# Optimization experiments

Measured on AMD Instinct MI355X. Metric: run time of the kernel, lower is better.

The kernel has to match this reference:

```python
import jax, jax.numpy as jnp
import numpy as np

B, T, LBL = 256, 1024, 128  # batch, seq_len, label_size (incl. start/end)
NUM = LBL - 2               # real emission labels


def setup_inputs() -> dict:
    key = jax.random.key(0)
    k1, k2, k3, k4 = jax.random.split(key, 4)
    logits = jax.random.normal(k1, (B, T, NUM), jnp.float32)
    labels = jax.random.randint(k2, (B, T), 0, NUM)
    lens = jax.random.randint(k3, (B,), 1, T + 1)  # 1..T inclusive
    transition = jax.random.normal(k4, (LBL, LBL), jnp.float32)
    # CRF.initialize(): nothing may transition INTO start-row source or OUT of end
    transition = transition.at[:, LBL - 1].set(-100.0)
    transition = transition.at[LBL - 2, :].set(-100.0)
    return {"logits": logits, "labels": labels, "lens": lens, "transition": transition}


def reference(logits, labels, lens, transition):
    """CRF negative-free log-likelihood pieces: returns gold_score - norm_score per sequence ([B])."""
    Bb, Tt, num = logits.shape
    L = transition.shape[0]
    start, end = L - 2, L - 1

    # pad_logits: append two -1000 columns for start/end labels -> [B, T, L]
    pads = jnp.full((Bb, Tt, 2), -1000.0, logits.dtype)
    lg = jnp.concatenate([logits, pads], axis=2)

    # ---- gold unary score ----
    mask_t = jnp.arange(Tt)[None, :] < lens[:, None]            # [B, T]
    unary = jnp.take_along_axis(lg, labels[..., None], axis=2)[..., 0]
    unary = jnp.where(mask_t, unary, 0.0).sum(axis=1)

    # ---- gold binary (transition) score ----
    ext = jnp.concatenate(
        [jnp.full((Bb, 1), start, labels.dtype), labels,
         jnp.full((Bb, 1), end, labels.dtype)], axis=1)          # [B, T+2]
    mask_e = jnp.arange(Tt + 2)[None, :] < (lens + 1)[:, None]
    ext = jnp.where(mask_e, ext, end)                            # positions >= len+1 -> end
    trn_scr = transition[ext[:, 1:], ext[:, :-1]]                # [B, T+1] (row=next, col=prev)
    mask_b = jnp.arange(Tt + 1)[None, :] < (lens + 1)[:, None]
    binary = jnp.where(mask_b, trn_scr, 0.0).sum(axis=1)

    gold = unary + binary

    # ---- partition (norm) score via log-sum-exp scan over time ----
    alpha0 = jnp.full((Bb, L), -100.0, lg.dtype).at[:, start].set(0.0)
    lg_t = jnp.transpose(lg, (1, 0, 2))                          # [T, B, L]

    def step(alpha, xs):
        logit, t = xs                                            # logit: [B, L]
        # mat[b, j, i] = logit[b, j] + alpha[b, i] + transition[j, i]
        mat = logit[:, :, None] + alpha[:, None, :] + transition[None]
        alpha_nxt = jax.nn.logsumexp(mat, axis=2)                # [B, L]
        alpha = jnp.where((t < lens)[:, None], alpha_nxt, alpha)
        return alpha, None

    alpha, _ = jax.lax.scan(step, alpha0, (lg_t, jnp.arange(Tt)))
    alpha = alpha + transition[end][None, :]
    norm = jax.nn.logsumexp(alpha, axis=1)                       # [B]

    return gold - norm
```

## Files before the change

### kernel.cpp

```cpp
#include <hip/hip_runtime.h>


typedef _Float16 half_t;
typedef _Float16 h2 __attribute__((ext_vector_type(2)));
typedef _Float16 h8 __attribute__((ext_vector_type(8)));

#define TB  1024
#define NUM 126
#define LBL 128

__device__ __forceinline__ float dot2(h2 a, h2 b, float c) {
  return __builtin_amdgcn_fdot2(a, b, c, false);
}

template <int U>
__device__ __forceinline__ float dotu(h8 a, h8 e, float c) {
  return dot2(__builtin_shufflevector(a, a, 2 * U, 2 * U + 1),
              __builtin_shufflevector(e, e, 2 * U, 2 * U + 1), c);
}

template <int CTRL>
__device__ __forceinline__ float dpp_max_step(float x) {
  int xi = __float_as_int(x);
  int yi = __builtin_amdgcn_update_dpp(xi, xi, CTRL, 0xF, 0xF, false);
  return fmaxf(x, __int_as_float(yi));
}

__device__ __forceinline__ float wave_max64(float x) {
  x = dpp_max_step<0x111>(x);
  x = dpp_max_step<0x112>(x);
  x = dpp_max_step<0x114>(x);
  x = dpp_max_step<0x118>(x);
  x = dpp_max_step<0x142>(x);
  x = dpp_max_step<0x143>(x);
  return __int_as_float(__builtin_amdgcn_readlane(__float_as_int(x), 63));
}

__global__ __launch_bounds__(64, 1)
void crf_fwd(const float* __restrict__ logits, const int* __restrict__ labels,
             const int* __restrict__ lens, const float* __restrict__ trans,
             float* __restrict__ out)
{
  const int b  = blockIdx.x;
  const int l  = threadIdx.x;
  const int j0 = l;
  const int j1 = l + 64;
  const int off1 = (j1 < NUM) ? j1 : (NUM - 1);
  const float mask1 = (j1 < NUM) ? 1.0f : 0.0f;
  const int len = lens[b];

  __shared__ h2 a_sh[64];
  h8* a_sh8 = (h8*)a_sh;

  const float* lgbase = logits + (size_t)b * TB * NUM;
  const int*   lab    = labels + (size_t)b * TB;

  h8 E0[16], E1[16];
  {
    const float* tr0 = trans + j0 * LBL;
    const float* tr1 = trans + j1 * LBL;
    #pragma unroll
    for (int q = 0; q < 16; ++q) {
      h8 v0, v1;
      #pragma unroll
      for (int e = 0; e < 8; ++e) {
        int p = 8 * q + e;
        int i = (p >> 1) + 64 * (p & 1);
        v0[e] = (half_t)__expf(tr0[i]);
        v1[e] = (half_t)__expf(tr1[i]);
      }
      E0[q] = v0; E1[q] = v1;
    }
  }

  float g = 0.f;
  #pragma unroll
  for (int kk = 0; kk < 16; ++kk) {
    int t = l + 64 * kk;
    if (t < len) {
      int lt = lab[t];
      int lp = (t == 0) ? (LBL - 2) : lab[t - 1];
      g += lgbase[(size_t)t * NUM + lt] + trans[lt * LBL + lp];
    }
  }
  if (l == 0) g += trans[(LBL - 1) * LBL + lab[len - 1]];
  #pragma unroll
  for (int o = 1; o < 64; o <<= 1) g += __shfl_xor(g, o);
  const float gold = g;

  {
    h2 a_init;
    a_init[0] = (half_t)0.0f;
    a_init[1] = (half_t)((j1 == LBL - 2) ? 1.0f : 0.0f);
    a_sh[l] = a_init;
  }

  float plg0[4], plg1[4];
  #pragma unroll
  for (int d = 0; d < 4; ++d) {
    plg0[d] = lgbase[(size_t)d * NUM + j0];
    plg1[d] = lgbase[(size_t)d * NUM + off1];
  }

  int   P    = 6;
  int   Kacc = 0;
  int   Kout = 0;
  float w0_out = 1.f, w1_out = 1.f;

#define STEP_BODY(Q0, Q1)                                                   \
  {                                                                         \
    float eL0 = __expf(Q0);                                                 \
    float eL1 = __expf(Q1) * mask1;                                         \
    float s0a = 0.f, s0b = 0.f, s1a = 0.f, s1b = 0.f;                       \
    _Pragma("unroll")                                                       \
    for (int q = 0; q < 16; q += 2) {                                       \
      h8 avA = a_sh8[q], avB = a_sh8[q + 1];    \
      h8 e0A = E0[q], e0B = E0[q + 1], e1A = E1[q], e1B = E1[q + 1];        \
      s0a = dotu<0>(avA, e0A, s0a);  s0b = dotu<0>(avB, e0B, s0b);          \
      s1a = dotu<0>(avA, e1A, s1a);  s1b = dotu<0>(avB, e1B, s1b);          \
      s0a = dotu<1>(avA, e0A, s0a);  s0b = dotu<1>(avB, e0B, s0b);          \
      s1a = dotu<1>(avA, e1A, s1a);  s1b = dotu<1>(avB, e1B, s1b);          \
      s0a = dotu<2>(avA, e0A, s0a);  s0b = dotu<2>(avB, e0B, s0b);          \
      s1a = dotu<2>(avA, e1A, s1a);  s1b = dotu<2>(avB, e1B, s1b);          \
      s0a = dotu<3>(avA, e0A, s0a);  s0b = dotu<3>(avB, e0B, s0b);          \
      s1a = dotu<3>(avA, e1A, s1a);  s1b = dotu<3>(avB, e1B, s1b);          \
    }                                                                       \
    float w0 = (s0a + s0b) * eL0;                                           \
    float w1 = (s1a + s1b) * eL1;                                           \
    float sc = __int_as_float((127 - P) << 23);      \
    h2 pk;                                                                  \
    pk[0] = (half_t)(w0 * sc);                                              \
    pk[1] = (half_t)(w1 * sc);                                              \
    a_sh[l] = pk;                        \
    Kout = Kacc;  Kacc += P;                           \
    \
    float m  = wave_max64(fmaxf(w0, w1));                                   \
    int   Em = ((__float_as_int(m) >> 23) & 0xFF) - 127;                    \
    P = Em - P + 6;                   \
    w0_out = w0; w1_out = w1;                                               \
  }

  int t = 0;
  for (; t + 4 <= len; t += 4) {
    int r0 = t + 4, r1 = t + 5, r2 = t + 6, r3 = t + 7;
    r0 = (r0 < TB) ? r0 : (TB - 1);  r1 = (r1 < TB) ? r1 : (TB - 1);
    r2 = (r2 < TB) ? r2 : (TB - 1);  r3 = (r3 < TB) ? r3 : (TB - 1);
    STEP_BODY(plg0[0], plg1[0])
    plg0[0] = lgbase[(size_t)r0 * NUM + j0];
    plg1[0] = lgbase[(size_t)r0 * NUM + off1];
    STEP_BODY(plg0[1], plg1[1])
    plg0[1] = lgbase[(size_t)r1 * NUM + j0];
    plg1[1] = lgbase[(size_t)r1 * NUM + off1];
    STEP_BODY(plg0[2], plg1[2])
    plg0[2] = lgbase[(size_t)r2 * NUM + j0];
    plg1[2] = lgbase[(size_t)r2 * NUM + off1];
    STEP_BODY(plg0[3], plg1[3])
    plg0[3] = lgbase[(size_t)r3 * NUM + j0];
    plg1[3] = lgbase[(size_t)r3 * NUM + off1];
  }
  const int rem = len - t;
  if (rem > 0) STEP_BODY(plg0[0], plg1[0])
  if (rem > 1) STEP_BODY(plg0[1], plg1[1])
  if (rem > 2) STEP_BODY(plg0[2], plg1[2])
#undef STEP_BODY

  const float LN2 = 0.6931471805599453f;
  float SigmaPrev = (float)Kout * LN2;
  float alpha0 = SigmaPrev + __logf(w0_out);
  float alpha1 = SigmaPrev + __logf(w1_out);

  float v0 = alpha0 + trans[(LBL - 1) * LBL + j0];
  float v1 = alpha1 + trans[(LBL - 1) * LBL + j1];
  float M = wave_max64(fmaxf(v0, v1));
  float p = __expf(v0 - M) + __expf(v1 - M);
  #pragma unroll
  for (int o = 1; o < 64; o <<= 1) p += __shfl_xor(p, o);
  if (l == 0) out[b] = gold - (M + __logf(p));
}

extern "C" void kernel_launch(void* const* d_in, const int* in_sizes, int n_in,
                              void* d_out, int out_size, void* d_ws, size_t ws_size,
                              hipStream_t stream) {
  const float* logits = (const float*)d_in[0];
  const int*   labels = (const int*)d_in[1];
  const int*   lens   = (const int*)d_in[2];
  const float* trans  = (const float*)d_in[3];
  float* out = (float*)d_out;
  (void)in_sizes; (void)n_in; (void)out_size; (void)d_ws; (void)ws_size;
  crf_fwd<<<256, 64, 0, stream>>>(logits, labels, lens, trans, out);
}
```

Baseline: 583.2 us.

## Split each sequence's CRF recurrence across four waves with double-buffered shared state

Each block now uses 256 threads (4 waves) instead of one wave. Each lane owns one output label and half of the source labels, and the two halves are combined with v_permlane32_swap. Alpha vectors and per-wave maxima are double-buffered in LDS with one barrier per time step. The rescale exponent is now derived from the previous step's cross-wave max, which takes the wave-max reduction off the critical path. The intent is to cut the per-step serial dot-product chain by spreading it over more lanes, at the cost of a block barrier every step and more LDS traffic.

```diff
diff --git a/kernel.cpp b/kernel.cpp
--- a/kernel.cpp
+++ b/kernel.cpp
@@ -9,14 +9,14 @@
 #define NUM 126
 #define LBL 128
 
-__device__ __forceinline__ float dot2(h2 a, h2 b, float c) {
+__device__ __forceinline__ float dot2f(h2 a, h2 b, float c) {
   return __builtin_amdgcn_fdot2(a, b, c, false);
 }
 
 template <int U>
 __device__ __forceinline__ float dotu(h8 a, h8 e, float c) {
-  return dot2(__builtin_shufflevector(a, a, 2 * U, 2 * U + 1),
-              __builtin_shufflevector(e, e, 2 * U, 2 * U + 1), c);
+  return dot2f(__builtin_shufflevector(a, a, 2 * U, 2 * U + 1),
+               __builtin_shufflevector(e, e, 2 * U, 2 * U + 1), c);
 }
 
 template <int CTRL>
@@ -26,156 +26,159 @@
   return fmaxf(x, __int_as_float(yi));
 }
 
-__device__ __forceinline__ float wave_max64(float x) {
+__device__ __forceinline__ float wave_max_tree(float x) {
   x = dpp_max_step<0x111>(x);
   x = dpp_max_step<0x112>(x);
   x = dpp_max_step<0x114>(x);
   x = dpp_max_step<0x118>(x);
   x = dpp_max_step<0x142>(x);
   x = dpp_max_step<0x143>(x);
-  return __int_as_float(__builtin_amdgcn_readlane(__float_as_int(x), 63));
+  return x;
 }
 
-__global__ __launch_bounds__(64, 1)
+__device__ __forceinline__ float wave_max64(float x) {
+  return __int_as_float(
+      __builtin_amdgcn_readlane(__float_as_int(wave_max_tree(x)), 63));
+}
+
+__device__ __forceinline__ float half_sum(float x) {
+  int a = __float_as_int(x), b = __float_as_int(x);
+  asm("v_permlane32_swap_b32 %0, %1" : "+v"(a), "+v"(b));
+  return __int_as_float(a) + __int_as_float(b);
+}
+
+__global__ __launch_bounds__(256, 1)
 void crf_fwd(const float* __restrict__ logits, const int* __restrict__ labels,
              const int* __restrict__ lens, const float* __restrict__ trans,
              float* __restrict__ out)
 {
-  const int b  = blockIdx.x;
-  const int l  = threadIdx.x;
-  const int j0 = l;
-  const int j1 = l + 64;
-  const int off1 = (j1 < NUM) ? j1 : (NUM - 1);
-  const float mask1 = (j1 < NUM) ? 1.0f : 0.0f;
-  const int len = lens[b];
+  const int b    = blockIdx.x;
+  const int tid  = threadIdx.x;
+  const int wid  = tid >> 6;
+  const int l    = tid & 63;
+  const int half = l >> 5;
+  const int r    = (wid << 5) + (l & 31);
+  const int rr   = (r < NUM) ? r : (NUM - 1);
+  const float rmask = (r < NUM) ? 1.0f : 0.0f;
+  const int len  = lens[b];
 
-  __shared__ h2 a_sh[64];
-  h8* a_sh8 = (h8*)a_sh;
+  __shared__ __align__(16) h2    a_sh[2][64];
+  __shared__ __align__(16) float maxsh[2][4];
+  __shared__ float goldsh[4], Msh[4], psh[4];
 
   const float* lgbase = logits + (size_t)b * TB * NUM;
   const int*   lab    = labels + (size_t)b * TB;
 
-  h8 E0[16], E1[16];
+  h8 E[8];
   {
-    const float* tr0 = trans + j0 * LBL;
-    const float* tr1 = trans + j1 * LBL;
+    const float* tr = trans + r * LBL + half * 64;
     #pragma unroll
-    for (int q = 0; q < 16; ++q) {
-      h8 v0, v1;
+    for (int q = 0; q < 8; ++q) {
+      h8 v;
       #pragma unroll
-      for (int e = 0; e < 8; ++e) {
-        int p = 8 * q + e;
-        int i = (p >> 1) + 64 * (p & 1);
-        v0[e] = (half_t)__expf(tr0[i]);
-        v1[e] = (half_t)__expf(tr1[i]);
-      }
-      E0[q] = v0; E1[q] = v1;
+      for (int e = 0; e < 8; ++e) v[e] = (half_t)__expf(tr[8 * q + e]);
+      E[q] = v;
     }
   }
 
   float g = 0.f;
   #pragma unroll
-  for (int kk = 0; kk < 16; ++kk) {
-    int t = l + 64 * kk;
+  for (int kk = 0; kk < 4; ++kk) {
+    int t = tid + 256 * kk;
     if (t < len) {
       int lt = lab[t];
       int lp = (t == 0) ? (LBL - 2) : lab[t - 1];
       g += lgbase[(size_t)t * NUM + lt] + trans[lt * LBL + lp];
     }
   }
-  if (l == 0) g += trans[(LBL - 1) * LBL + lab[len - 1]];
+  if (tid == 0) g += trans[(LBL - 1) * LBL + lab[len - 1]];
   #pragma unroll
   for (int o = 1; o < 64; o <<= 1) g += __shfl_xor(g, o);
-  const float gold = g;
+  if (l == 0) goldsh[wid] = g;
 
-  {
-    h2 a_init;
-    a_init[0] = (half_t)0.0f;
-    a_init[1] = (half_t)((j1 == LBL - 2) ? 1.0f : 0.0f);
-    a_sh[l] = a_init;
+  if (tid < 64) {
+    h2 ai;
+    ai[0] = (half_t)((2 * tid     == LBL - 2) ? 1.0f : 0.0f);
+    ai[1] = (half_t)((2 * tid + 1 == LBL - 2) ? 1.0f : 0.0f);
+    a_sh[0][tid] = ai;
   }
+  if (tid < 8) maxsh[tid >> 2][tid & 3] = 64.0f;
+  __syncthreads();
 
-  float plg0[4], plg1[4];
+  float plg[4];
   #pragma unroll
-  for (int d = 0; d < 4; ++d) {
-    plg0[d] = lgbase[(size_t)d * NUM + j0];
-    plg1[d] = lgbase[(size_t)d * NUM + off1];
-  }
+  for (int d = 0; d < 4; ++d) plg[d] = lgbase[(size_t)d * NUM + rr];
 
-  int   P    = 6;
-  int   Kacc = 0;
-  int   Kout = 0;
-  float w0_out = 1.f, w1_out = 1.f;
+  int P = 6, Kacc = 0, Kout = 0, par = 0;
+  float w_out = 1.f;
 
-#define STEP_BODY(Q0, Q1)                                                   \
+#define STEP_BODY(Q)                                                        \
   {                                                                         \
-    float eL0 = __expf(Q0);                                                 \
-    float eL1 = __expf(Q1) * mask1;                                         \
-    float s0a = 0.f, s0b = 0.f, s1a = 0.f, s1b = 0.f;                       \
+       \
+    const float4 mv = *(const float4*)(&maxsh[par][0]);                     \
+    const h8* ap = (const h8*)(&a_sh[par][0]) + half * 8;                   \
+    float eL = __expf(Q) * rmask;                                           \
+    float s0 = 0.f, s1 = 0.f, s2 = 0.f, s3 = 0.f;                           \
     _Pragma("unroll")                                                       \
-    for (int q = 0; q < 16; q += 2) {                                       \
-      h8 avA = a_sh8[q], avB = a_sh8[q + 1];    \
-      h8 e0A = E0[q], e0B = E0[q + 1], e1A = E1[q], e1B = E1[q + 1];        \
-      s0a = dotu<0>(avA, e0A, s0a);  s0b = dotu<0>(avB, e0B, s0b);          \
-      s1a = dotu<0>(avA, e1A, s1a);  s1b = dotu<0>(avB, e1B, s1b);          \
-      s0a = dotu<1>(avA, e0A, s0a);  s0b = dotu<1>(avB, e0B, s0b);          \
-      s1a = dotu<1>(avA, e1A, s1a);  s1b = dotu<1>(avB, e1B, s1b);          \
-      s0a = dotu<2>(avA, e0A, s0a);  s0b = dotu<2>(avB, e0B, s0b);          \
-      s1a = dotu<2>(avA, e1A, s1a);  s1b = dotu<2>(avB, e1B, s1b);          \
-      s0a = dotu<3>(avA, e0A, s0a);  s0b = dotu<3>(avB, e0B, s0b);          \
-      s1a = dotu<3>(avA, e1A, s1a);  s1b = dotu<3>(avB, e1B, s1b);          \
+    for (int q = 0; q < 8; q += 2) {                                        \
+      h8 avA = ap[q], avB = ap[q + 1];                                      \
+      h8 eA = E[q], eB = E[q + 1];                                          \
+      s0 = dotu<0>(avA, eA, s0);  s1 = dotu<1>(avA, eA, s1);                \
+      s2 = dotu<2>(avA, eA, s2);  s3 = dotu<3>(avA, eA, s3);                \
+      s0 = dotu<0>(avB, eB, s0);  s1 = dotu<1>(avB, eB, s1);                \
+      s2 = dotu<2>(avB, eB, s2);  s3 = dotu<3>(avB, eB, s3);                \
     }                                                                       \
-    float w0 = (s0a + s0b) * eL0;                                           \
-    float w1 = (s1a + s1b) * eL1;                                           \
-    float sc = __int_as_float((127 - P) << 23);      \
-    h2 pk;                                                                  \
-    pk[0] = (half_t)(w0 * sc);                                              \
-    pk[1] = (half_t)(w1 * sc);                                              \
-    a_sh[l] = pk;                        \
+    float mm = fmaxf(fmaxf(mv.x, mv.y), fmaxf(mv.z, mv.w));                 \
+    P = (((__float_as_int(mm) >> 23) & 0xFF) - 127) - P + 6;                \
+         \
+    float ssum = half_sum((s0 + s1) + (s2 + s3));                           \
+    float w = ssum * eL;                                                    \
+    float sc = __int_as_float((127 - P) << 23);            \
+    ((half_t*)(&a_sh[par ^ 1][0]))[r] = (half_t)(w * sc);    \
     Kout = Kacc;  Kacc += P;                           \
-    \
-    float m  = wave_max64(fmaxf(w0, w1));                                   \
-    int   Em = ((__float_as_int(m) >> 23) & 0xFF) - 127;                    \
-    P = Em - P + 6;                   \
-    w0_out = w0; w1_out = w1;                                               \
+    float m = wave_max_tree(w);                                             \
+    if (l == 63) maxsh[par ^ 1][wid] = m;                                   \
+            \
+    asm volatile("s_waitcnt lgkmcnt(0)\n\ts_barrier" ::: "memory");         \
+    w_out = w;  par ^= 1;                                                   \
   }
 
   int t = 0;
   for (; t + 4 <= len; t += 4) {
-    int r0 = t + 4, r1 = t + 5, r2 = t + 6, r3 = t + 7;
-    r0 = (r0 < TB) ? r0 : (TB - 1);  r1 = (r1 < TB) ? r1 : (TB - 1);
-    r2 = (r2 < TB) ? r2 : (TB - 1);  r3 = (r3 < TB) ? r3 : (TB - 1);
-    STEP_BODY(plg0[0], plg1[0])
-    plg0[0] = lgbase[(size_t)r0 * NUM + j0];
-    plg1[0] = lgbase[(size_t)r0 * NUM + off1];
-    STEP_BODY(plg0[1], plg1[1])
-    plg0[1] = lgbase[(size_t)r1 * NUM + j0];
-    plg1[1] = lgbase[(size_t)r1 * NUM + off1];
-    STEP_BODY(plg0[2], plg1[2])
-    plg0[2] = lgbase[(size_t)r2 * NUM + j0];
-    plg1[2] = lgbase[(size_t)r2 * NUM + off1];
-    STEP_BODY(plg0[3], plg1[3])
-    plg0[3] = lgbase[(size_t)r3 * NUM + j0];
-    plg1[3] = lgbase[(size_t)r3 * NUM + off1];
+    int q0 = t + 4, q1 = t + 5, q2 = t + 6, q3 = t + 7;
+    q0 = (q0 < TB) ? q0 : (TB - 1);  q1 = (q1 < TB) ? q1 : (TB - 1);
+    q2 = (q2 < TB) ? q2 : (TB - 1);  q3 = (q3 < TB) ? q3 : (TB - 1);
+    STEP_BODY(plg[0])
+    plg[0] = lgbase[(size_t)q0 * NUM + rr];
+    STEP_BODY(plg[1])
+    plg[1] = lgbase[(size_t)q1 * NUM + rr];
+    STEP_BODY(plg[2])
+    plg[2] = lgbase[(size_t)q2 * NUM + rr];
+    STEP_BODY(plg[3])
+    plg[3] = lgbase[(size_t)q3 * NUM + rr];
   }
   const int rem = len - t;
-  if (rem > 0) STEP_BODY(plg0[0], plg1[0])
-  if (rem > 1) STEP_BODY(plg0[1], plg1[1])
-  if (rem > 2) STEP_BODY(plg0[2], plg1[2])
+  if (rem > 0) STEP_BODY(plg[0])
+  if (rem > 1) STEP_BODY(plg[1])
+  if (rem > 2) STEP_BODY(plg[2])
 #undef STEP_BODY
 
   const float LN2 = 0.6931471805599453f;
-  float SigmaPrev = (float)Kout * LN2;
-  float alpha0 = SigmaPrev + __logf(w0_out);
-  float alpha1 = SigmaPrev + __logf(w1_out);
-
-  float v0 = alpha0 + trans[(LBL - 1) * LBL + j0];
-  float v1 = alpha1 + trans[(LBL - 1) * LBL + j1];
-  float M = wave_max64(fmaxf(v0, v1));
-  float p = __expf(v0 - M) + __expf(v1 - M);
+  float v = (float)Kout * LN2 + __logf(w_out) + trans[(LBL - 1) * LBL + r];
+  if (half) v = -__builtin_inff();
+  float M = wave_max64(v);
+  float p = __expf(v - M);
   #pragma unroll
   for (int o = 1; o < 64; o <<= 1) p += __shfl_xor(p, o);
-  if (l == 0) out[b] = gold - (M + __logf(p));
+  if (l == 0) { Msh[wid] = M; psh[wid] = p; }
+  __syncthreads();
+  if (tid == 0) {
+    float gT = goldsh[0] + goldsh[1] + goldsh[2] + goldsh[3];
+    float Mg = fmaxf(fmaxf(Msh[0], Msh[1]), fmaxf(Msh[2], Msh[3]));
+    float pg = psh[0] * __expf(Msh[0] - Mg) + psh[1] * __expf(Msh[1] - Mg)
+             + psh[2] * __expf(Msh[2] - Mg) + psh[3] * __expf(Msh[3] - Mg);
+    out[b] = gT - (Mg + __logf(pg));
+  }
 }
 
 extern "C" void kernel_launch(void* const* d_in, const int* in_sizes, int n_in,
@@ -187,5 +190,5 @@
   const float* trans  = (const float*)d_in[3];
   float* out = (float*)d_out;
   (void)in_sizes; (void)n_in; (void)out_size; (void)d_ws; (void)ws_size;
-  crf_fwd<<<256, 64, 0, stream>>>(logits, labels, lens, trans, out);
+  crf_fwd<<<256, 256, 0, stream>>>(logits, labels, lens, trans, out);
 }
```

Measured after the change: 485.5 us. 1.2x faster.

## Broadcast alpha via cross-lane permutes instead of LDS in CRF scan

Applied to the files above, without the earlier changes.

Alpha values no longer go through shared memory each step. They are broadcast to all lanes with permlane32_swap, ds_swizzle and DPP row rotations, and the transition exponentials are pre-permuted to match the rotated lane order. Each lane now owns two adjacent labels (2l, 2l+1), so the emission logits are read with one float2 load. The goal is to cut LDS write/read latency and the implicit barrier from the serial per-timestep critical path, at the cost of many DPP/swizzle ops per step and higher register use.

```diff
diff --git a/kernel.cpp b/kernel.cpp
--- a/kernel.cpp
+++ b/kernel.cpp
@@ -3,20 +3,25 @@
 
 typedef _Float16 half_t;
 typedef _Float16 h2 __attribute__((ext_vector_type(2)));
-typedef _Float16 h8 __attribute__((ext_vector_type(8)));
 
 #define TB  1024
 #define NUM 126
 #define LBL 128
 
-__device__ __forceinline__ float dot2(h2 a, h2 b, float c) {
+__device__ __forceinline__ float dot2f(h2 a, h2 b, float c) {
   return __builtin_amdgcn_fdot2(a, b, c, false);
 }
 
-template <int U>
-__device__ __forceinline__ float dotu(h8 a, h8 e, float c) {
-  return dot2(__builtin_shufflevector(a, a, 2 * U, 2 * U + 1),
-              __builtin_shufflevector(e, e, 2 * U, 2 * U + 1), c);
+__device__ __forceinline__ h2 bits_h2(int x) {
+  union { int i; h2 h; } u; u.i = x; return u.h;
+}
+__device__ __forceinline__ int h2_bits(h2 h) {
+  union { int i; h2 h; } u; u.h = h; return u.i;
+}
+
+template <int N>
+__device__ __forceinline__ int ror(int x) {
+  return __builtin_amdgcn_update_dpp(x, x, 0x120 | N, 0xF, 0xF, false);
 }
 
 template <int CTRL>
@@ -36,6 +41,27 @@
   return __int_as_float(__builtin_amdgcn_readlane(__float_as_int(x), 63));
 }
 
+__device__ __forceinline__ void base4(int cur, int g[4]) {
+  int g0 = cur, g1 = cur;
+  asm("v_permlane32_swap_b32 %0, %1" : "+v"(g0), "+v"(g1));
+  g[0] = g0;
+  g[1] = g1;
+  g[2] = __builtin_amdgcn_ds_swizzle(g0, 0x401F);
+  g[3] = __builtin_amdgcn_ds_swizzle(g1, 0x401F);
+}
+
+__device__ __forceinline__ void expand16(int base, int rr[16]) {
+  rr[0]  = base;
+  rr[1]  = ror<1>(rr[0]);
+  rr[2]  = ror<2>(rr[0]);  rr[3]  = ror<2>(rr[1]);
+  rr[4]  = ror<4>(rr[0]);  rr[5]  = ror<4>(rr[1]);
+  rr[6]  = ror<4>(rr[2]);  rr[7]  = ror<4>(rr[3]);
+  rr[8]  = ror<8>(rr[0]);  rr[9]  = ror<8>(rr[1]);
+  rr[10] = ror<8>(rr[2]);  rr[11] = ror<8>(rr[3]);
+  rr[12] = ror<8>(rr[4]);  rr[13] = ror<8>(rr[5]);
+  rr[14] = ror<8>(rr[6]);  rr[15] = ror<8>(rr[7]);
+}
+
 __global__ __launch_bounds__(64, 1)
 void crf_fwd(const float* __restrict__ logits, const int* __restrict__ labels,
              const int* __restrict__ lens, const float* __restrict__ trans,
@@ -43,33 +69,37 @@
 {
   const int b  = blockIdx.x;
   const int l  = threadIdx.x;
-  const int j0 = l;
-  const int j1 = l + 64;
-  const int off1 = (j1 < NUM) ? j1 : (NUM - 1);
-  const float mask1 = (j1 < NUM) ? 1.0f : 0.0f;
+  const int r0 = 2 * l;
+  const int r1 = 2 * l + 1;
+  const float rm0 = (r0 < NUM) ? 1.0f : 0.0f;
+  const float rm1 = (r1 < NUM) ? 1.0f : 0.0f;
+  const int cl  = (r1 < NUM) ? r0 : (NUM - 2);
   const int len = lens[b];
-
-  __shared__ h2 a_sh[64];
-  h8* a_sh8 = (h8*)a_sh;
 
   const float* lgbase = logits + (size_t)b * TB * NUM;
   const int*   lab    = labels + (size_t)b * TB;
 
-  h8 E0[16], E1[16];
+  h2 E0[64], E1[64];
   {
-    const float* tr0 = trans + j0 * LBL;
-    const float* tr1 = trans + j1 * LBL;
+    int g[4];
+    base4(l, g);
+    const float* t0 = trans + r0 * LBL;
+    const float* t1 = trans + r1 * LBL;
     #pragma unroll
-    for (int q = 0; q < 16; ++q) {
-      h8 v0, v1;
-      #pragma unroll
-      for (int e = 0; e < 8; ++e) {
-        int p = 8 * q + e;
-        int i = (p >> 1) + 64 * (p & 1);
-        v0[e] = (half_t)__expf(tr0[i]);
-        v1[e] = (half_t)__expf(tr1[i]);
-      }
-      E0[q] = v0; E1[q] = v1;
+    for (int v = 0; v < 4; ++v) {
+      int rr[16];
+      expand16(g[v], rr);
+      #pragma unroll
+      for (int k = 0; k < 16; ++k) {
+        int s = rr[k];
+        h2 e0, e1;
+        e0[0] = (half_t)__expf(t0[2 * s]);
+        e0[1] = (half_t)__expf(t0[2 * s + 1]);
+        e1[0] = (half_t)__expf(t1[2 * s]);
+        e1[1] = (half_t)__expf(t1[2 * s + 1]);
+        E0[16 * v + k] = e0;
+        E1[16 * v + k] = e1;
+      }
     }
   }
 
@@ -88,89 +118,98 @@
   for (int o = 1; o < 64; o <<= 1) g += __shfl_xor(g, o);
   const float gold = g;
 
-  {
-    h2 a_init;
-    a_init[0] = (half_t)0.0f;
-    a_init[1] = (half_t)((j1 == LBL - 2) ? 1.0f : 0.0f);
-    a_sh[l] = a_init;
-  }
-
-  float plg0[4], plg1[4];
-  #pragma unroll
-  for (int d = 0; d < 4; ++d) {
-    plg0[d] = lgbase[(size_t)d * NUM + j0];
-    plg1[d] = lgbase[(size_t)d * NUM + off1];
-  }
-
-  int   P    = 6;
-  int   Kacc = 0;
-  int   Kout = 0;
+  h2 a_init;
+  a_init[0] = (half_t)((r0 == LBL - 2) ? 1.0f : 0.0f);
+  a_init[1] = (half_t)0.0f;
+  int   cur = h2_bits(a_init);
+  int   P = 6, Kacc = 0, Kout = 0;
   float w0_out = 1.f, w1_out = 1.f;
 
-#define STEP_BODY(Q0, Q1)                                                   \
-  {                                                                         \
-    float eL0 = __expf(Q0);                                                 \
-    float eL1 = __expf(Q1) * mask1;                                         \
-    float s0a = 0.f, s0b = 0.f, s1a = 0.f, s1b = 0.f;                       \
-    _Pragma("unroll")                                                       \
-    for (int q = 0; q < 16; q += 2) {                                       \
-      h8 avA = a_sh8[q], avB = a_sh8[q + 1];    \
-      h8 e0A = E0[q], e0B = E0[q + 1], e1A = E1[q], e1B = E1[q + 1];        \
-      s0a = dotu<0>(avA, e0A, s0a);  s0b = dotu<0>(avB, e0B, s0b);          \
-      s1a = dotu<0>(avA, e1A, s1a);  s1b = dotu<0>(avB, e1B, s1b);          \
-      s0a = dotu<1>(avA, e0A, s0a);  s0b = dotu<1>(avB, e0B, s0b);          \
-      s1a = dotu<1>(avA, e1A, s1a);  s1b = dotu<1>(avB, e1B, s1b);          \
-      s0a = dotu<2>(avA, e0A, s0a);  s0b = dotu<2>(avB, e0B, s0b);          \
-      s1a = dotu<2>(avA, e1A, s1a);  s1b = dotu<2>(avB, e1B, s1b);          \
-      s0a = dotu<3>(avA, e0A, s0a);  s0b = dotu<3>(avB, e0B, s0b);          \
-      s1a = dotu<3>(avA, e1A, s1a);  s1b = dotu<3>(avB, e1B, s1b);          \
-    }                                                                       \
-    float w0 = (s0a + s0b) * eL0;                                           \
-    float w1 = (s1a + s1b) * eL1;                                           \
-    float sc = __int_as_float((127 - P) << 23);      \
-    h2 pk;                                                                  \
-    pk[0] = (half_t)(w0 * sc);                                              \
-    pk[1] = (half_t)(w1 * sc);                                              \
-    a_sh[l] = pk;                        \
-    Kout = Kacc;  Kacc += P;                           \
-    \
-    float m  = wave_max64(fmaxf(w0, w1));                                   \
-    int   Em = ((__float_as_int(m) >> 23) & 0xFF) - 127;                    \
-    P = Em - P + 6;                   \
-    w0_out = w0; w1_out = w1;                                               \
-  }
+  float2 plg[4];
+  #pragma unroll
+  for (int d = 0; d < 4; ++d)
+    plg[d] = *(const float2*)(lgbase + (size_t)d * NUM + cl);
+
+  auto step = [&](float2 Qv) __attribute__((always_inline)) {
+    int gq[4];
+    base4(cur, gq);
+    float eL0 = __expf(Qv.x) * rm0;
+    float eL1 = __expf(Qv.y) * rm1;
+    float a0 = 0.f, a1 = 0.f, a2 = 0.f, a3 = 0.f;
+    float b0 = 0.f, b1 = 0.f, b2 = 0.f, b3 = 0.f;
+    {
+      int rr[16];
+      expand16(gq[0], rr);
+      #pragma unroll
+      for (int k = 0; k < 16; ++k) {
+        h2 x = bits_h2(rr[k]);
+        a0 = dot2f(x, E0[k], a0);  b0 = dot2f(x, E1[k], b0);
+      }
+    }
+    {
+      int rr[16];
+      expand16(gq[1], rr);
+      #pragma unroll
+      for (int k = 0; k < 16; ++k) {
+        h2 x = bits_h2(rr[k]);
+        a1 = dot2f(x, E0[16 + k], a1);  b1 = dot2f(x, E1[16 + k], b1);
+      }
+    }
+    {
+      int rr[16];
+      expand16(gq[2], rr);
+      #pragma unroll
+      for (int k = 0; k < 16; ++k) {
+        h2 x = bits_h2(rr[k]);
+        a2 = dot2f(x, E0[32 + k], a2);  b2 = dot2f(x, E1[32 + k], b2);
+      }
+    }
+    {
+      int rr[16];
+      expand16(gq[3], rr);
+      #pragma unroll
+      for (int k = 0; k < 16; ++k) {
+        h2 x = bits_h2(rr[k]);
+        a3 = dot2f(x, E0[48 + k], a3);  b3 = dot2f(x, E1[48 + k], b3);
+      }
+    }
+    float w0 = ((a0 + a1) + (a2 + a3)) * eL0;
+    float w1 = ((b0 + b1) + (b2 + b3)) * eL1;
+    float sc = __int_as_float((127 - P) << 23);
+    h2 pk;
+    pk[0] = (half_t)(w0 * sc);
+    pk[1] = (half_t)(w1 * sc);
+    cur = h2_bits(pk);
+    Kout = Kacc;  Kacc += P;
+    float m  = wave_max64(fmaxf(w0, w1));
+    int   Em = ((__float_as_int(m) >> 23) & 0xFF) - 127;
+    P = Em - P + 6;
+    w0_out = w0;  w1_out = w1;
+  };
 
   int t = 0;
   for (; t + 4 <= len; t += 4) {
-    int r0 = t + 4, r1 = t + 5, r2 = t + 6, r3 = t + 7;
-    r0 = (r0 < TB) ? r0 : (TB - 1);  r1 = (r1 < TB) ? r1 : (TB - 1);
-    r2 = (r2 < TB) ? r2 : (TB - 1);  r3 = (r3 < TB) ? r3 : (TB - 1);
-    STEP_BODY(plg0[0], plg1[0])
-    plg0[0] = lgbase[(size_t)r0 * NUM + j0];
-    plg1[0] = lgbase[(size_t)r0 * NUM + off1];
-    STEP_BODY(plg0[1], plg1[1])
-    plg0[1] = lgbase[(size_t)r1 * NUM + j0];
-    plg1[1] = lgbase[(size_t)r1 * NUM + off1];
-    STEP_BODY(plg0[2], plg1[2])
-    plg0[2] = lgbase[(size_t)r2 * NUM + j0];
-    plg1[2] = lgbase[(size_t)r2 * NUM + off1];
-    STEP_BODY(plg0[3], plg1[3])
-    plg0[3] = lgbase[(size_t)r3 * NUM + j0];
-    plg1[3] = lgbase[(size_t)r3 * NUM + off1];
+    int q0 = t + 4, q1 = t + 5, q2 = t + 6, q3 = t + 7;
+    q0 = (q0 < TB) ? q0 : (TB - 1);  q1 = (q1 < TB) ? q1 : (TB - 1);
+    q2 = (q2 < TB) ? q2 : (TB - 1);  q3 = (q3 < TB) ? q3 : (TB - 1);
+    step(plg[0]);
+    plg[0] = *(const float2*)(lgbase + (size_t)q0 * NUM + cl);
+    step(plg[1]);
+    plg[1] = *(const float2*)(lgbase + (size_t)q1 * NUM + cl);
+    step(plg[2]);
+    plg[2] = *(const float2*)(lgbase + (size_t)q2 * NUM + cl);
+    step(plg[3]);
+    plg[3] = *(const float2*)(lgbase + (size_t)q3 * NUM + cl);
   }
   const int rem = len - t;
-  if (rem > 0) STEP_BODY(plg0[0], plg1[0])
-  if (rem > 1) STEP_BODY(plg0[1], plg1[1])
-  if (rem > 2) STEP_BODY(plg0[2], plg1[2])
-#undef STEP_BODY
+  if (rem > 0) step(plg[0]);
+  if (rem > 1) step(plg[1]);
+  if (rem > 2) step(plg[2]);
 
   const float LN2 = 0.6931471805599453f;
-  float SigmaPrev = (float)Kout * LN2;
-  float alpha0 = SigmaPrev + __logf(w0_out);
-  float alpha1 = SigmaPrev + __logf(w1_out);
-
-  float v0 = alpha0 + trans[(LBL - 1) * LBL + j0];
-  float v1 = alpha1 + trans[(LBL - 1) * LBL + j1];
+  float K = (float)Kout * LN2;
+  float v0 = K + __logf(w0_out) + trans[(LBL - 1) * LBL + r0];
+  float v1 = K + __logf(w1_out) + trans[(LBL - 1) * LBL + r1];
   float M = wave_max64(fmaxf(v0, v1));
   float p = __expf(v0 - M) + __expf(v1 - M);
   #pragma unroll
```

Result: slower. 738.1 us (+26.6%).
